# Optimization experiments

Measured on AMD Instinct MI355X. Metric: run time of the kernel, lower is better.

## Reference

```python
import jax, jax.numpy as jnp
import numpy as np

N, E, CS, HE, H = 10000, 160000, 128, 32, 4
S0, V1 = 16, 8          # feat_irreps = 16x0e + 8x1o
QK0, QK1 = 4, 2         # qk_irreps per head = 4x0e + 2x1o
VO0, VO1 = 4, 4         # v_irreps  per head = 4x0e + 4x1o
OK0, OK1 = QK0 * H, QK1 * H     # 16, 8
OV0, OV1 = VO0 * H, VO1 * H     # 16, 16
K_NUMEL = S0*OK0 + V1*OK0 + S0*OK1 + V1*OK1 + V1*OK1   # 640
V_NUMEL = S0*OV0 + V1*OV0 + S0*OV1 + V1*OV1 + V1*OV1   # 896
EPS = 1e-5


def _tp(fs, fv, sh_s, sh_v, w, o0, o1):
    """CG tensor product of (s0 scalars + v1 vectors) with sh=(1x0e+1x1o),
    per-edge weights w (shared_weights=False); outputs o0 scalars + o1 vectors.
    Paths: 0e*0e->0e, 1o.1o->0e (dot), 0e*1o->1o, 1o*0e->1o, 1o x 1o->1o (cross)."""
    s0, v1 = fs.shape[-1], fv.shape[-2]
    i = 0
    ws = []
    for (a, b) in ((s0, o0), (v1, o0), (s0, o1), (v1, o1), (v1, o1)):
        ws.append(w[:, i:i + a * b].reshape(-1, a, b)); i += a * b
    wA, wB, wC, wD, wE = ws
    c0a = jnp.einsum('eu,euw->ew', fs * sh_s[:, None], wA) / np.sqrt(s0)
    dv = jnp.einsum('eui,ei->eu', fv, sh_v)
    c0b = jnp.einsum('eu,euw->ew', dv, wB) / np.sqrt(v1)
    out0 = (c0a + c0b) / np.sqrt(2.0)
    c1c = jnp.einsum('eu,euw->ew', fs, wC)[:, :, None] * sh_v[:, None, :] / np.sqrt(s0)
    c1d = jnp.einsum('eui,euw->ewi', fv, wD) * sh_s[:, None, None] / np.sqrt(v1)
    crs = jnp.cross(fv, sh_v[:, None, :])
    c1e = jnp.einsum('eui,euw->ewi', crs, wE) / np.sqrt(v1)
    out1 = (c1c + c1d + c1e) / np.sqrt(3.0)
    return out0, out1


def _forward(frame_features, rigid_rot, rigid_trans, tfn_features, edge_features, edge_sh,
             W_f0, b_f0, W_f1, b_f1, Wg_s, Wg_v, Wq_s, Wq_v,
             Wk1, bk1, Wk2, bk2, Wv1, bv1, Wv2, bv2,
             Wo_s, Wo_v, Ws_s, Ws_v, bn_ws, bn_bs, bn_wv, edge_index):
    dst, src = edge_index[0], edge_index[1]
    n = tfn_features.shape[0]
    tfn_s = tfn_features[:, :S0]
    tfn_v = tfn_features[:, S0:].reshape(n, V1, 3)
    sh_s, sh_v = edge_sh[:, 0], edge_sh[:, 1:4]

    # frame -> irrep features: 0e via Linear, 1o via Linear + rigid apply
    f0 = frame_features @ W_f0 + b_f0                                   # [N, S0*H]
    f1 = (frame_features @ W_f1 + b_f1).reshape(n, V1 * H, 3)
    f1 = jnp.einsum('nij,nuj->nui', rigid_rot, f1) + rigid_trans[:, None, :]
    gs = f0 @ Wg_s / np.sqrt(f0.shape[-1])                              # o3.Linear 0e -> [N, S0]
    gv = jnp.einsum('nui,uw->nwi', f1, Wg_v) / np.sqrt(f1.shape[1])     # o3.Linear 1o -> [N, V1, 3]

    # queries per node, per head
    q_s = (tfn_s @ Wq_s / np.sqrt(S0)).reshape(n, H, QK0)
    q_v = (jnp.einsum('nui,uw->nwi', tfn_v, Wq_v) / np.sqrt(V1)).reshape(n, H, QK1, 3)

    # per-edge dynamic TP weights from edge features (the big memory term)
    kw = jax.nn.relu(edge_features @ Wk1 + bk1) @ Wk2 + bk2             # [E, 640]
    vw = jax.nn.relu(edge_features @ Wv1 + bv1) @ Wv2 + bv2             # [E, 896]

    fs, fv = gs[dst], gv[dst]                                           # gather at edge_dst
    k_s, k_v = _tp(fs, fv, sh_s, sh_v, kw, OK0, OK1)
    v_s, v_v = _tp(fs, fv, sh_s, sh_v, vw, OV0, OV1)
    k_s = k_s.reshape(-1, H, QK0); k_v = k_v.reshape(-1, H, QK1, 3)
    v_s = v_s.reshape(-1, H, VO0); v_v = v_v.reshape(-1, H, VO1, 3)

    # attention scores + segment softmax over edge_src groups
    attn = jnp.einsum('ehj,ehj->eh', q_s[src], k_s) + jnp.einsum('ehji,ehji->eh', q_v[src], k_v)
    m = jax.ops.segment_max(attn, src, num_segments=n)
    ex = jnp.exp(attn - m[src])
    den = jax.ops.segment_sum(ex, src, num_segments=n)
    alpha = ex / (den[src] + 1e-9)

    upd_s = jax.ops.segment_sum(v_s * alpha[..., None], src, num_segments=n).reshape(n, OV0)
    upd_v = jax.ops.segment_sum(v_v * alpha[..., None, None], src, num_segments=n).reshape(n, OV1, 3)

    out_s = upd_s @ Wo_s / np.sqrt(OV0) + tfn_s @ Ws_s / np.sqrt(S0)
    out_v = jnp.einsum('nui,uw->nwi', upd_v, Wo_v) / np.sqrt(OV1) \
          + jnp.einsum('nui,uw->nwi', tfn_v, Ws_v) / np.sqrt(V1)

    # e3nn-style BatchNorm: scalars mean/var normalized, vectors norm normalized
    mu = out_s.mean(0); xc = out_s - mu
    out_s = xc / jnp.sqrt((xc * xc).mean(0) + EPS) * bn_ws + bn_bs
    n2 = (out_v * out_v).sum(-1).mean(0)
    out_v = out_v / jnp.sqrt(n2 + EPS)[None, :, None] * bn_wv[None, :, None]

    return jnp.concatenate([out_s, out_v.reshape(n, V1 * 3)], axis=-1)   # [N, 40]


def setup_inputs():
    key = jax.random.key(0)
    ks = iter(jax.random.split(key, 40))
    rn = lambda *s: jax.random.normal(next(ks), s, dtype=jnp.float32)
    return dict(
        frame_features=rn(N, CS),
        rigid_rot=rn(N, 3, 3),
        rigid_trans=rn(N, 3),
        tfn_features=rn(N, S0 + 3 * V1),
        edge_features=rn(E, HE),
        edge_sh=rn(E, 4),
        edge_index=jax.random.randint(next(ks), (2, E), 0, N, dtype=jnp.int32),
        W_f0=rn(CS, S0 * H) / np.sqrt(CS), b_f0=jnp.zeros((S0 * H,), jnp.float32),
        W_f1=rn(CS, V1 * H * 3) / np.sqrt(CS), b_f1=jnp.zeros((V1 * H * 3,), jnp.float32),
        Wg_s=rn(S0 * H, S0), Wg_v=rn(V1 * H, V1),
        Wq_s=rn(S0, QK0 * H), Wq_v=rn(V1, QK1 * H),
        Wk1=rn(HE, HE) / np.sqrt(HE), bk1=jnp.zeros((HE,), jnp.float32),
        Wk2=rn(HE, K_NUMEL) / np.sqrt(HE), bk2=jnp.zeros((K_NUMEL,), jnp.float32),
        Wv1=rn(HE, HE) / np.sqrt(HE), bv1=jnp.zeros((HE,), jnp.float32),
        Wv2=rn(HE, V_NUMEL) / np.sqrt(HE), bv2=jnp.zeros((V_NUMEL,), jnp.float32),
        Wo_s=rn(VO0 * H, S0), Wo_v=rn(VO1 * H, V1),
        Ws_s=rn(S0, S0), Ws_v=rn(V1, V1),
        bn_ws=jnp.ones((S0,), jnp.float32), bn_bs=jnp.zeros((S0,), jnp.float32),
        bn_wv=jnp.ones((V1,), jnp.float32),
    )


def reference(frame_features, rigid_rot, rigid_trans, tfn_features, edge_features, edge_sh, edge_index,
              W_f0, b_f0, W_f1, b_f1, Wg_s, Wg_v, Wq_s, Wq_v,
              Wk1, bk1, Wk2, bk2, Wv1, bv1, Wv2, bv2,
              Wo_s, Wo_v, Ws_s, Ws_v, bn_ws, bn_bs, bn_wv):
    return _forward(frame_features, rigid_rot, rigid_trans, tfn_features, edge_features, edge_sh,
                    W_f0, b_f0, W_f1, b_f1, Wg_s, Wg_v, Wq_s, Wq_v,
                    Wk1, bk1, Wk2, bk2, Wv1, bv1, Wv2, bv2,
                    Wo_s, Wo_v, Ws_s, Ws_v, bn_ws, bn_bs, bn_wv, edge_index)
```

## Files before the change

### kernel.cpp

```cpp
#include <hip/hip_runtime.h>
#include <hip/hip_bf16.h>
#include <math.h>

#define NN 10000
#define EE 160000
#define CSZ 128

#define INV_S8  0.35355339059327373f
#define INV_S32 0.17677669529663687f
#define INV_S2  0.7071067811865476f
#define INV_S3  0.5773502691896258f

typedef short s16x8 __attribute__((ext_vector_type(8)));
typedef float f32x4 __attribute__((ext_vector_type(4)));

__device__ __forceinline__ unsigned short f2bf(float f){
  __hip_bfloat16 h = __float2bfloat16(f);
  return *reinterpret_cast<unsigned short*>(&h);
}

__global__ __launch_bounds__(256) void k_f0f1(
    const float* __restrict__ frame,
    const float* __restrict__ Wf0, const float* __restrict__ bf0,
    const float* __restrict__ Wf1, const float* __restrict__ bf1,
    float* __restrict__ f0f1){
  int lane = threadIdx.x & 63, wave = threadIdx.x >> 6;
  int c = blockIdx.x*64 + lane;
  int n0 = blockIdx.y*16 + wave*4;
  if(c >= 160) return;
  bool is0 = c < 64;
  int cc = is0 ? c : (c-64);
  const float* W = is0 ? Wf0 : Wf1;
  int ldw = is0 ? 64 : 96;
  float b = is0 ? bf0[cc] : bf1[cc];
  float acc[4] = {b, b, b, b};
  const float* fp = frame + (size_t)n0*CSZ;
  #pragma unroll 4
  for(int k=0;k<CSZ;k++){
    float w = W[k*ldw + cc];
    #pragma unroll
    for(int j=0;j<4;j++)
      acc[j] = fmaf(fp[j*CSZ + k], w, acc[j]);
  }
  #pragma unroll
  for(int j=0;j<4;j++) f0f1[(size_t)(n0+j)*160 + c] = acc[j];
}

__global__ __launch_bounds__(256) void k_node2(
    const float* __restrict__ f0f1, const float* __restrict__ rot,
    const float* __restrict__ trans, const float* __restrict__ tfn,
    const float* __restrict__ Wgs, const float* __restrict__ Wgv,
    const float* __restrict__ Wqs, const float* __restrict__ Wqv,
    float* __restrict__ Gs, float* __restrict__ Gv,
    float* __restrict__ Qs, float* __restrict__ Qv){
  __shared__ float f1r[4][32][3];
  int ln = threadIdx.x & 63;
  int g  = threadIdx.x >> 6;
  int n  = blockIdx.x*4 + g;
  if(n < NN && ln < 32){
    int u = ln;
    float v0 = f0f1[(size_t)n*160 + 64 + u*3 + 0];
    float v1 = f0f1[(size_t)n*160 + 64 + u*3 + 1];
    float v2 = f0f1[(size_t)n*160 + 64 + u*3 + 2];
    const float* R = rot + (size_t)n*9;
    const float* t = trans + (size_t)n*3;
    f1r[g][u][0] = R[0]*v0 + R[1]*v1 + R[2]*v2 + t[0];
    f1r[g][u][1] = R[3]*v0 + R[4]*v1 + R[5]*v2 + t[1];
    f1r[g][u][2] = R[6]*v0 + R[7]*v1 + R[8]*v2 + t[2];
  }
  __syncthreads();
  if(n >= NN) return;
  if(ln < 16){
    int w = ln; float a = 0.f;
    for(int u=0;u<64;u++) a = fmaf(f0f1[(size_t)n*160+u], Wgs[u*16+w], a);
    Gs[(size_t)n*16+w] = a * 0.125f;
  } else if(ln < 40){
    int idx = ln-16, w = idx/3, i = idx%3; float a = 0.f;
    for(int u=0;u<32;u++) a = fmaf(f1r[g][u][i], Wgv[u*8+w], a);
    Gv[(size_t)n*24+idx] = a * INV_S32;
  }
  if(ln < 16){
    int w = ln; float a = 0.f;
    for(int u=0;u<16;u++) a = fmaf(tfn[(size_t)n*40+u], Wqs[u*16+w], a);
    Qs[(size_t)n*16+w] = a * 0.25f;
  } else if(ln < 40){
    int idx = ln-16, w = idx/3, i = idx%3; float a = 0.f;
    for(int u=0;u<8;u++) a = fmaf(tfn[(size_t)n*40+16+u*3+i], Wqv[u*8+w], a);
    Qv[(size_t)n*24+idx] = a * INV_S8;
  }
}

__global__ __launch_bounds__(256) void k_hist(const int* __restrict__ ei, int* __restrict__ cnt){
  int e = blockIdx.x*256 + threadIdx.x;
  if(e < EE) atomicAdd(&cnt[ei[EE + e]], 1);
}

__global__ __launch_bounds__(256) void k_scan(const int* __restrict__ cnt,
                                              int* __restrict__ ofs, int* __restrict__ fill){
  __shared__ int tsum[256];
  int t = threadIdx.x;
  const int CH = (NN + 255)/256;
  int base = t*CH;
  int s = 0;
  for(int i=0;i<CH;i++){ int idx=base+i; if(idx<NN) s += cnt[idx]; }
  tsum[t] = s;
  __syncthreads();
  for(int off=1; off<256; off<<=1){
    int v = (t>=off)? tsum[t-off] : 0;
    __syncthreads();
    tsum[t] += v;
    __syncthreads();
  }
  int run = (t==0)? 0 : tsum[t-1];
  for(int i=0;i<CH;i++){
    int idx = base+i;
    if(idx < NN){ ofs[idx] = run; fill[idx] = run; run += cnt[idx]; }
  }
  if(t==255) ofs[NN] = tsum[255];
}

__global__ __launch_bounds__(256) void k_scatter(const int* __restrict__ ei,
                                                 int* __restrict__ fill, int* __restrict__ elist){
  int e = blockIdx.x*256 + threadIdx.x;
  if(e >= EE) return;
  int src = ei[EE + e];
  int pos = atomicAdd(&fill[src], 1);
  elist[pos] = e;
}

__global__ __launch_bounds__(256) void k_prepw(
    const float* __restrict__ Wk2, const float* __restrict__ bk2,
    const float* __restrict__ Wv2, const float* __restrict__ bv2,
    unsigned short* __restrict__ A2rK, unsigned short* __restrict__ A2rV,
    float* __restrict__ biasK, float* __restrict__ biasV){
  int tid = blockIdx.x*256 + threadIdx.x;
  const int NV = 896*32, NK = 640*32;
  if(tid < NV){
    int c = tid>>5, h = tid&31;
    float s = (c<384)? INV_S2 : INV_S3;
    A2rV[(c>>4)*512 + (c&15)*32 + h] = f2bf(Wv2[h*896+c]*s);
  } else if(tid < NV+NK){
    int i = tid - NV; int c = i>>5, h = i&31;
    float s = (c<384)? INV_S2 : INV_S3;
    A2rK[(c>>4)*512 + (c&15)*32 + h] = f2bf(Wk2[h*640+c]*s);
  } else if(tid < NV+NK+896){
    int c = tid - (NV+NK);
    biasV[c] = bv2[c] * ((c<384)? INV_S2 : INV_S3);
  } else if(tid < NV+NK+896+640){
    int c = tid - (NV+NK+896);
    biasK[c] = bk2[c] * ((c<384)? INV_S2 : INV_S3);
  }
}

#define HID_TO_FRAGS(W1, b1) { \
  unsigned short* hL = (unsigned short*)&F[0][0]; \
  float efv[32]; \
  const float4* efp = (const float4*)(ef + (size_t)e*32); \
  _Pragma("unroll") \
  for(int q=0;q<8;q++){ float4 t=efp[q]; efv[q*4]=t.x; efv[q*4+1]=t.y; efv[q*4+2]=t.z; efv[q*4+3]=t.w; } \
  float hd[32]; \
  _Pragma("unroll") \
  for(int h=0;h<32;h++) hd[h] = b1[h]; \
  _Pragma("unroll") \
  for(int k=0;k<32;k++){ \
    float ekv = efv[k]; \
    _Pragma("unroll") \
    for(int h=0;h<32;h++) hd[h] = fmaf(ekv, W1[k*32+h], hd[h]); \
  } \
  _Pragma("unroll") \
  for(int gg=0;gg<4;gg++){ \
    s16x8 p; \
    _Pragma("unroll") \
    for(int j=0;j<8;j++) p[j] = (short)f2bf(fmaxf(hd[gg*8+j], 0.f)); \
    *(s16x8*)&hL[((g*4+gg)*16 + e16)*8] = p; \
  } \
  _Pragma("unroll") \
  for(int tt=0;tt<4;tt++) \
    af[tt] = *(const s16x8*)&hL[((tt*4 + g)*16 + e16)*8]; }

#define STAGE_FEATURES() { \
  const float4* g4 = (const float4*)(Gs + (size_t)dst*16); \
  _Pragma("unroll") \
  for(int q=0;q<4;q++){ float4 t = g4[q]; \
    F[q*4+0][lane]=t.x*0.25f; F[q*4+1][lane]=t.y*0.25f; \
    F[q*4+2][lane]=t.z*0.25f; F[q*4+3][lane]=t.w*0.25f; } \
  const float4* v4 = (const float4*)(Gv + (size_t)dst*24); \
  _Pragma("unroll") \
  for(int q=0;q<6;q++){ float4 t = v4[q]; \
    F[16+q*4+0][lane]=t.x; F[16+q*4+1][lane]=t.y; \
    F[16+q*4+2][lane]=t.z; F[16+q*4+3][lane]=t.w; } \
  _Pragma("unroll") \
  for(int tt=0;tt<4;tt++){ \
    int sl = tt*16 + e16; \
    shs_t[tt]  = __shfl(shs, sl); \
    sv_t[tt][0]= __shfl(sv0, sl); \
    sv_t[tt][1]= __shfl(sv1, sl); \
    sv_t[tt][2]= __shfl(sv2, sl); \
    shsI8_t[tt]= shs_t[tt]*INV_S8; \
  } }

#define NTILE_MFMA(A2r, bias, NT) \
  s16x8 Aw = *(const s16x8*)&A2r[(NT)*512 + e16*32 + g*8]; \
  float4 b4 = *(const float4*)&bias[(NT)*16 + g*4]; \
  f32x4 acc4[4]; \
  _Pragma("unroll") \
  for(int tt=0; tt<4; ++tt){ \
    f32x4 a0 = {b4.x, b4.y, b4.z, b4.w}; \
    acc4[tt] = __builtin_amdgcn_mfma_f32_16x16x32_bf16(Aw, af[tt], a0, 0, 0, 0); \
  }

__global__ __launch_bounds__(128) void k_edge_v3(
    const int* __restrict__ ei, const float* __restrict__ esh,
    const float* __restrict__ ef,
    const float* __restrict__ Gs, const float* __restrict__ Gv,
    const float* __restrict__ Wv1, const float* __restrict__ bv1,
    const unsigned short* __restrict__ A2rV, const float* __restrict__ biasV,
    float* __restrict__ EdgeV){
  __shared__ float featAll[2][40][64];
  int wave = threadIdx.x >> 6, lane = threadIdx.x & 63;
  float (*F)[64] = featAll[wave];
  int ebase = blockIdx.x*128 + wave*64;
  int e = ebase + lane;
  int e16 = lane & 15, g = lane >> 4;

  int dst = ei[e];
  float4 sh4 = *(const float4*)(esh + (size_t)e*4);
  float shs = sh4.x, sv0 = sh4.y, sv1 = sh4.z, sv2 = sh4.w;

  s16x8 af[4];
  HID_TO_FRAGS(Wv1, bv1);
  float shs_t[4], sv_t[4][3], shsI8_t[4];
  STAGE_FEATURES();

  float A16[4][4] = {};
  #pragma unroll 1
  for(int ntile=0; ntile<16; ++ntile){
    NTILE_MFMA(A2rV, biasV, ntile);
    #pragma unroll
    for(int tt=0; tt<4; ++tt){
      float f = F[ntile][tt*16+e16] * shs_t[tt];
      #pragma unroll
      for(int r=0;r<4;r++) A16[tt][r] = fmaf(f, acc4[tt][r], A16[tt][r]);
    }
  }
  #pragma unroll 1
  for(int ntile=16; ntile<24; ++ntile){
    NTILE_MFMA(A2rV, biasV, ntile);
    int u3 = 16 + (ntile-16)*3;
    #pragma unroll
    for(int tt=0; tt<4; ++tt){
      int eL = tt*16+e16;
      float f = (F[u3+0][eL]*sv_t[tt][0] + F[u3+1][eL]*sv_t[tt][1]
               + F[u3+2][eL]*sv_t[tt][2]) * INV_S8;
      #pragma unroll
      for(int r=0;r<4;r++) A16[tt][r] = fmaf(f, acc4[tt][r], A16[tt][r]);
    }
  }
  #pragma unroll
  for(int tt=0; tt<4; ++tt){
    int eo = ebase + tt*16 + e16;
    *(float4*)(EdgeV + (size_t)eo*64 + g*4) =
        make_float4(A16[tt][0], A16[tt][1], A16[tt][2], A16[tt][3]);
  }

  float VV[4][4][3] = {};
  #pragma unroll 1
  for(int ntile=24; ntile<40; ++ntile){
    NTILE_MFMA(A2rV, biasV, ntile);
    #pragma unroll
    for(int tt=0; tt<4; ++tt){
      float f = F[ntile-24][tt*16+e16];
      #pragma unroll
      for(int r=0;r<4;r++){
        float c = f*acc4[tt][r];
        VV[tt][r][0] = fmaf(c, sv_t[tt][0], VV[tt][r][0]);
        VV[tt][r][1] = fmaf(c, sv_t[tt][1], VV[tt][r][1]);
        VV[tt][r][2] = fmaf(c, sv_t[tt][2], VV[tt][r][2]);
      }
    }
  }
  #pragma unroll 1
  for(int ntile=40; ntile<48; ++ntile){
    NTILE_MFMA(A2rV, biasV, ntile);
    int u3 = 16 + (ntile-40)*3;
    #pragma unroll
    for(int tt=0; tt<4; ++tt){
      int eL = tt*16+e16;
      float f0 = F[u3+0][eL]*shsI8_t[tt];
      float f1 = F[u3+1][eL]*shsI8_t[tt];
      float f2 = F[u3+2][eL]*shsI8_t[tt];
      #pragma unroll
      for(int r=0;r<4;r++){
        VV[tt][r][0] = fmaf(f0, acc4[tt][r], VV[tt][r][0]);
        VV[tt][r][1] = fmaf(f1, acc4[tt][r], VV[tt][r][1]);
        VV[tt][r][2] = fmaf(f2, acc4[tt][r], VV[tt][r][2]);
      }
    }
  }
  #pragma unroll 1
  for(int ntile=48; ntile<56; ++ntile){
    NTILE_MFMA(A2rV, biasV, ntile);
    int u3 = 16 + (ntile-48)*3;
    #pragma unroll
    for(int tt=0; tt<4; ++tt){
      int eL = tt*16+e16;
      float a0 = F[u3+0][eL], a1 = F[u3+1][eL], a2 = F[u3+2][eL];
      float x0 = (a1*sv_t[tt][2] - a2*sv_t[tt][1])*INV_S8;
      float x1 = (a2*sv_t[tt][0] - a0*sv_t[tt][2])*INV_S8;
      float x2 = (a0*sv_t[tt][1] - a1*sv_t[tt][0])*INV_S8;
      #pragma unroll
      for(int r=0;r<4;r++){
        VV[tt][r][0] = fmaf(x0, acc4[tt][r], VV[tt][r][0]);
        VV[tt][r][1] = fmaf(x1, acc4[tt][r], VV[tt][r][1]);
        VV[tt][r][2] = fmaf(x2, acc4[tt][r], VV[tt][r][2]);
      }
    }
  }
  #pragma unroll
  for(int tt=0; tt<4; ++tt){
    int eo = ebase + tt*16 + e16;
    float* op = EdgeV + (size_t)eo*64 + 16 + g*12;
    float v[12] = {VV[tt][0][0],VV[tt][0][1],VV[tt][0][2],
                   VV[tt][1][0],VV[tt][1][1],VV[tt][1][2],
                   VV[tt][2][0],VV[tt][2][1],VV[tt][2][2],
                   VV[tt][3][0],VV[tt][3][1],VV[tt][3][2]};
    #pragma unroll
    for(int k=0;k<6;k++)
      *(float2*)(op + k*2) = make_float2(v[k*2], v[k*2+1]);
  }
}

__global__ __launch_bounds__(128) void k_edge_k3(
    const int* __restrict__ ei, const float* __restrict__ esh,
    const float* __restrict__ ef,
    const float* __restrict__ Gs, const float* __restrict__ Gv,
    const float* __restrict__ Qs, const float* __restrict__ Qv,
    const float* __restrict__ Wk1, const float* __restrict__ bk1,
    const unsigned short* __restrict__ A2rK, const float* __restrict__ biasK,
    float* __restrict__ Attn){
  __shared__ float featAll[2][40][64];
  int wave = threadIdx.x >> 6, lane = threadIdx.x & 63;
  float (*F)[64] = featAll[wave];
  int ebase = blockIdx.x*128 + wave*64;
  int e = ebase + lane;
  int e16 = lane & 15, g = lane >> 4;

  int dst = ei[e];
  float4 sh4 = *(const float4*)(esh + (size_t)e*4);
  float shs = sh4.x, sv0 = sh4.y, sv1 = sh4.z, sv2 = sh4.w;

  s16x8 af[4];
  HID_TO_FRAGS(Wk1, bk1);
  float shs_t[4], sv_t[4][3], shsI8_t[4];
  STAGE_FEATURES();

  float KS[4][4] = {};
  #pragma unroll 1
  for(int ntile=0; ntile<16; ++ntile){
    NTILE_MFMA(A2rK, biasK, ntile);
    #pragma unroll
    for(int tt=0; tt<4; ++tt){
      float f = F[ntile][tt*16+e16] * shs_t[tt];
      #pragma unroll
      for(int r=0;r<4;r++) KS[tt][r] = fmaf(f, acc4[tt][r], KS[tt][r]);
    }
  }
  #pragma unroll 1
  for(int ntile=16; ntile<24; ++ntile){
    NTILE_MFMA(A2rK, biasK, ntile);
    int u3 = 16 + (ntile-16)*3;
    #pragma unroll
    for(int tt=0; tt<4; ++tt){
      int eL = tt*16+e16;
      float f = (F[u3+0][eL]*sv_t[tt][0] + F[u3+1][eL]*sv_t[tt][1]
               + F[u3+2][eL]*sv_t[tt][2]) * INV_S8;
      #pragma unroll
      for(int r=0;r<4;r++) KS[tt][r] = fmaf(f, acc4[tt][r], KS[tt][r]);
    }
  }
  int src_t[4]; float ksd[4];
  #pragma unroll
  for(int tt=0; tt<4; ++tt){
    int eo = ebase + tt*16 + e16;
    src_t[tt] = ei[EE + eo];
    float4 q4 = *(const float4*)(Qs + (size_t)src_t[tt]*16 + g*4);
    ksd[tt] = q4.x*KS[tt][0] + q4.y*KS[tt][1] + q4.z*KS[tt][2] + q4.w*KS[tt][3];
  }

  float KV[4][4][3] = {};
  int gh = g >> 1;
  #pragma unroll 1
  for(int ntile=24; ntile<32; ++ntile){
    NTILE_MFMA(A2rK, biasK, ntile);
    int fr = (ntile-24)*2 + gh;
    #pragma unroll
    for(int tt=0; tt<4; ++tt){
      float f = F[fr][tt*16+e16];
      #pragma unroll
      for(int r=0;r<4;r++){
        float c = f*acc4[tt][r];
        KV[tt][r][0] = fmaf(c, sv_t[tt][0], KV[tt][r][0]);
        KV[tt][r][1] = fmaf(c, sv_t[tt][1], KV[tt][r][1]);
        KV[tt][r][2] = fmaf(c, sv_t[tt][2], KV[tt][r][2]);
      }
    }
  }
  #pragma unroll 1
  for(int ntile=32; ntile<36; ++ntile){
    NTILE_MFMA(A2rK, biasK, ntile);
    int u3 = 16 + ((ntile-32)*2 + gh)*3;
    #pragma unroll
    for(int tt=0; tt<4; ++tt){
      int eL = tt*16+e16;
      float f0 = F[u3+0][eL]*shsI8_t[tt];
      float f1 = F[u3+1][eL]*shsI8_t[tt];
      float f2 = F[u3+2][eL]*shsI8_t[tt];
      #pragma unroll
      for(int r=0;r<4;r++){
        KV[tt][r][0] = fmaf(f0, acc4[tt][r], KV[tt][r][0]);
        KV[tt][r][1] = fmaf(f1, acc4[tt][r], KV[tt][r][1]);
        KV[tt][r][2] = fmaf(f2, acc4[tt][r], KV[tt][r][2]);
      }
    }
  }
  #pragma unroll 1
  for(int ntile=36; ntile<40; ++ntile){
    NTILE_MFMA(A2rK, biasK, ntile);
    int u3 = 16 + ((ntile-36)*2 + gh)*3;
    #pragma unroll
    for(int tt=0; tt<4; ++tt){
      int eL = tt*16+e16;
      float a0 = F[u3+0][eL], a1 = F[u3+1][eL], a2 = F[u3+2][eL];
      float x0 = (a1*sv_t[tt][2] - a2*sv_t[tt][1])*INV_S8;
      float x1 = (a2*sv_t[tt][0] - a0*sv_t[tt][2])*INV_S8;
      float x2 = (a0*sv_t[tt][1] - a1*sv_t[tt][0])*INV_S8;
      #pragma unroll
      for(int r=0;r<4;r++){
        KV[tt][r][0] = fmaf(x0, acc4[tt][r], KV[tt][r][0]);
        KV[tt][r][1] = fmaf(x1, acc4[tt][r], KV[tt][r][1]);
        KV[tt][r][2] = fmaf(x2, acc4[tt][r], KV[tt][r][2]);
      }
    }
  }
  int godd = g & 1;
  #pragma unroll
  for(int tt=0; tt<4; ++tt){
    const float* qvp = Qv + (size_t)src_t[tt]*24 + godd*12;
    float4 qa = *(const float4*)(qvp);
    float4 qb = *(const float4*)(qvp+4);
    float4 qc = *(const float4*)(qvp+8);
    float kvs0 = qa.x*KV[tt][0][0] + qa.y*KV[tt][0][1] + qa.z*KV[tt][0][2]
               + qa.w*KV[tt][1][0] + qb.x*KV[tt][1][1] + qb.y*KV[tt][1][2];
    float kvs1 = qb.z*KV[tt][2][0] + qb.w*KV[tt][2][1] + qc.x*KV[tt][2][2]
               + qc.y*KV[tt][3][0] + qc.z*KV[tt][3][1] + qc.w*KV[tt][3][2];
    float p0 = ((g==0)? ksd[tt] : 0.f) + (godd? 0.f : kvs0);
    float p1 = ((g==1)? ksd[tt] : 0.f) + (godd? 0.f : kvs1);
    float p2 = ((g==2)? ksd[tt] : 0.f) + (godd? kvs0 : 0.f);
    float p3 = ((g==3)? ksd[tt] : 0.f) + (godd? kvs1 : 0.f);
    p0 += __shfl_xor(p0,16); p0 += __shfl_xor(p0,32);
    p1 += __shfl_xor(p1,16); p1 += __shfl_xor(p1,32);
    p2 += __shfl_xor(p2,16); p2 += __shfl_xor(p2,32);
    p3 += __shfl_xor(p3,16); p3 += __shfl_xor(p3,32);
    if(lane < 16){
      int eo = ebase + tt*16 + lane;
      *(float4*)(Attn + (size_t)eo*4) = make_float4(p0, p1, p2, p3);
    }
  }
}

__global__ __launch_bounds__(256) void k_reduce(
    const int* __restrict__ ofs, const int* __restrict__ elist,
    const float* __restrict__ Attn, const float* __restrict__ EdgeV,
    float* __restrict__ Upd){
  int wid = threadIdx.x >> 6, ln = threadIdx.x & 63;
  int n = blockIdx.x*4 + wid;
  if(n >= NN) return;
  int beg = ofs[n], end = ofs[n+1];
  float m0=-3.4e38f, m1=-3.4e38f, m2=-3.4e38f, m3=-3.4e38f;
  for(int i=beg+ln; i<end; i+=64){
    int e = elist[i];
    float4 a = *(const float4*)(Attn + (size_t)e*4);
    m0=fmaxf(m0,a.x); m1=fmaxf(m1,a.y); m2=fmaxf(m2,a.z); m3=fmaxf(m3,a.w);
  }
  #pragma unroll
  for(int off=1; off<64; off<<=1){
    m0=fmaxf(m0,__shfl_xor(m0,off)); m1=fmaxf(m1,__shfl_xor(m1,off));
    m2=fmaxf(m2,__shfl_xor(m2,off)); m3=fmaxf(m3,__shfl_xor(m3,off));
  }
  int h = (ln < 16) ? (ln >> 2) : (((ln - 16)/3) >> 2);
  float mh = (h==0)?m0:(h==1)?m1:(h==2)?m2:m3;
  float acc = 0.f, den = 0.f;
  for(int i=beg; i<end; i++){
    int e = elist[i];
    float v  = EdgeV[(size_t)e*64 + ln];
    float a  = Attn[(size_t)e*4 + h];
    float ex = __expf(a - mh);
    acc = fmaf(ex, v, acc);
    den += ex;
  }
  Upd[(size_t)n*64 + ln] = acc / (den + 1e-9f);
}

__global__ __launch_bounds__(256) void k_nodeout(
    const float* __restrict__ Upd, const float* __restrict__ tfn,
    const float* __restrict__ Wos, const float* __restrict__ Wov,
    const float* __restrict__ Wss, const float* __restrict__ Wsv,
    float* __restrict__ Pre, float* __restrict__ Stats){
  int n = blockIdx.x*256 + threadIdx.x;
  int lane = threadIdx.x & 63;
  float os[16], ov[24];
  if(n < NN){
    float us[16];
    #pragma unroll
    for(int u=0;u<16;u++) us[u] = Upd[(size_t)n*64+u];
    float uv[48];
    #pragma unroll
    for(int j=0;j<48;j++) uv[j] = Upd[(size_t)n*64+16+j];
    float ts[16];
    #pragma unroll
    for(int u=0;u<16;u++) ts[u] = tfn[(size_t)n*40+u];
    #pragma unroll
    for(int w=0;w<16;w++){
      float a=0.f, b=0.f;
      #pragma unroll
      for(int u=0;u<16;u++){ a = fmaf(us[u], Wos[u*16+w], a); b = fmaf(ts[u], Wss[u*16+w], b); }
      os[w] = (a + b)*0.25f;
    }
    float tv[24];
    #pragma unroll
    for(int j=0;j<24;j++) tv[j] = tfn[(size_t)n*40+16+j];
    #pragma unroll
    for(int w=0;w<8;w++){
      #pragma unroll
      for(int i=0;i<3;i++){
        float a=0.f;
        #pragma unroll
        for(int u=0;u<16;u++) a = fmaf(uv[u*3+i], Wov[u*8+w], a);
        float b=0.f;
        #pragma unroll
        for(int u=0;u<8;u++) b = fmaf(tv[u*3+i], Wsv[u*8+w], b);
        ov[w*3+i] = a*0.25f + b*INV_S8;
      }
    }
    float* p = Pre + (size_t)n*40;
    #pragma unroll
    for(int w=0;w<16;w++) p[w] = os[w];
    #pragma unroll
    for(int j=0;j<24;j++) p[16+j] = ov[j];
  } else {
    #pragma unroll
    for(int w=0;w<16;w++) os[w]=0.f;
    #pragma unroll
    for(int j=0;j<24;j++) ov[j]=0.f;
  }
#define WAVE_RED_ADD(v) { v += __shfl_xor(v,1); v += __shfl_xor(v,2); v += __shfl_xor(v,4); \
                          v += __shfl_xor(v,8); v += __shfl_xor(v,16); v += __shfl_xor(v,32); }
  #pragma unroll
  for(int c=0;c<16;c++){
    float s = os[c];       WAVE_RED_ADD(s);
    float q = os[c]*os[c]; WAVE_RED_ADD(q);
    if(lane==0){ atomicAdd(&Stats[c], s); atomicAdd(&Stats[16+c], q); }
  }
  #pragma unroll
  for(int w=0;w<8;w++){
    float q = ov[w*3]*ov[w*3] + ov[w*3+1]*ov[w*3+1] + ov[w*3+2]*ov[w*3+2];
    WAVE_RED_ADD(q);
    if(lane==0) atomicAdd(&Stats[32+w], q);
  }
#undef WAVE_RED_ADD
}

__global__ __launch_bounds__(256) void k_final(
    const float* __restrict__ Pre, const float* __restrict__ Stats,
    const float* __restrict__ bnws, const float* __restrict__ bnbs,
    const float* __restrict__ bnwv, float* __restrict__ Out){
  int idx = blockIdx.x*256 + threadIdx.x;
  if(idx >= NN*40) return;
  int n = idx/40, c = idx - n*40;
  float x = Pre[idx];
  float r;
  if(c < 16){
    float mu  = Stats[c]    * (1.f/NN);
    float var = Stats[16+c] * (1.f/NN) - mu*mu;
    r = (x - mu) / sqrtf(var + 1e-5f) * bnws[c] + bnbs[c];
  } else {
    int w = (c-16)/3;
    float n2 = Stats[32+w] * (1.f/NN);
    r = x / sqrtf(n2 + 1e-5f) * bnwv[w];
  }
  Out[idx] = r;
}

extern "C" void kernel_launch(void* const* d_in, const int* in_sizes, int n_in,
                              void* d_out, int out_size, void* d_ws, size_t ws_size,
                              hipStream_t stream){
  const float* frame = (const float*)d_in[0];
  const float* rot   = (const float*)d_in[1];
  const float* trans = (const float*)d_in[2];
  const float* tfn   = (const float*)d_in[3];
  const float* ef    = (const float*)d_in[4];
  const float* esh   = (const float*)d_in[5];
  const int*   ei    = (const int*)  d_in[6];
  const float* Wf0   = (const float*)d_in[7];
  const float* bf0   = (const float*)d_in[8];
  const float* Wf1   = (const float*)d_in[9];
  const float* bf1   = (const float*)d_in[10];
  const float* Wgs   = (const float*)d_in[11];
  const float* Wgv   = (const float*)d_in[12];
  const float* Wqs   = (const float*)d_in[13];
  const float* Wqv   = (const float*)d_in[14];
  const float* Wk1   = (const float*)d_in[15];
  const float* bk1   = (const float*)d_in[16];
  const float* Wk2   = (const float*)d_in[17];
  const float* bk2   = (const float*)d_in[18];
  const float* Wv1   = (const float*)d_in[19];
  const float* bv1   = (const float*)d_in[20];
  const float* Wv2   = (const float*)d_in[21];
  const float* bv2   = (const float*)d_in[22];
  const float* Wos   = (const float*)d_in[23];
  const float* Wov   = (const float*)d_in[24];
  const float* Wss   = (const float*)d_in[25];
  const float* Wsv   = (const float*)d_in[26];
  const float* bnws  = (const float*)d_in[27];
  const float* bnbs  = (const float*)d_in[28];
  const float* bnwv  = (const float*)d_in[29];

  float* ws   = (float*)d_ws;
  float* f0f1 = ws;
  float* Gs   = f0f1 + (size_t)NN*160;
  float* Gv   = Gs   + (size_t)NN*16;
  float* Qs   = Gv   + (size_t)NN*24;
  float* Qv   = Qs   + (size_t)NN*16;
  float* Attn = Qv   + (size_t)NN*24;
  float* Pre  = Attn + (size_t)EE*4;
  float* Upd  = Pre  + (size_t)NN*40;
  float* EdgeV= Upd  + (size_t)NN*64;
  float* Stats= EdgeV+ (size_t)EE*64;
  int*   cnt  = (int*)(Stats + 64);
  int*   ofs  = cnt + (NN+16);
  int*   fill = ofs + (NN+16);
  int*   elist= fill + (NN+16);
  float* biasV= (float*)(elist + EE);
  float* biasK= biasV + 896;
  unsigned short* A2rV = (unsigned short*)(biasK + 640);
  unsigned short* A2rK = A2rV + 896*32;

  hipMemsetAsync(Stats, 0, (64 + NN + 16)*sizeof(int), stream);

  k_f0f1    <<<dim3(3, NN/16),        256, 0, stream>>>(frame, Wf0, bf0, Wf1, bf1, f0f1);
  k_prepw   <<<dim3(198),             256, 0, stream>>>(Wk2, bk2, Wv2, bv2, A2rK, A2rV, biasK, biasV);
  k_node2   <<<dim3(NN/4),            256, 0, stream>>>(f0f1, rot, trans, tfn, Wgs, Wgv, Wqs, Wqv, Gs, Gv, Qs, Qv);
  k_hist    <<<dim3((EE+255)/256),    256, 0, stream>>>(ei, cnt);
  k_scan    <<<dim3(1),               256, 0, stream>>>(cnt, ofs, fill);
  k_scatter <<<dim3((EE+255)/256),    256, 0, stream>>>(ei, fill, elist);
  k_edge_v3 <<<dim3(EE/128),          128, 0, stream>>>(ei, esh, ef, Gs, Gv, Wv1, bv1, A2rV, biasV, EdgeV);
  k_edge_k3 <<<dim3(EE/128),          128, 0, stream>>>(ei, esh, ef, Gs, Gv, Qs, Qv, Wk1, bk1, A2rK, biasK, Attn);
  k_reduce  <<<dim3((NN+3)/4),        256, 0, stream>>>(ofs, elist, Attn, EdgeV, Upd);
  k_nodeout <<<dim3((NN+255)/256),    256, 0, stream>>>(Upd, tfn, Wos, Wov, Wss, Wsv, Pre, Stats);
  k_final   <<<dim3((NN*40+255)/256), 256, 0, stream>>>(Pre, Stats, bnws, bnbs, bnwv, (float*)d_out);
}
```

Measured before the change: 302.2 us.

## Parallelize node output projection across lanes per output channel with LDS staging

```diff
diff --git a/kernel.cpp b/kernel.cpp
--- a/kernel.cpp
+++ b/kernel.cpp
@@ -506,68 +506,65 @@
     const float* __restrict__ Wos, const float* __restrict__ Wov,
     const float* __restrict__ Wss, const float* __restrict__ Wsv,
     float* __restrict__ Pre, float* __restrict__ Stats){
-  int n = blockIdx.x*256 + threadIdx.x;
-  int lane = threadIdx.x & 63;
-  float os[16], ov[24];
-  if(n < NN){
-    float us[16];
-    #pragma unroll
-    for(int u=0;u<16;u++) us[u] = Upd[(size_t)n*64+u];
-    float uv[48];
-    #pragma unroll
-    for(int j=0;j<48;j++) uv[j] = Upd[(size_t)n*64+16+j];
-    float ts[16];
-    #pragma unroll
-    for(int u=0;u<16;u++) ts[u] = tfn[(size_t)n*40+u];
-    #pragma unroll
-    for(int w=0;w<16;w++){
+  __shared__ float sbuf[4][104];
+  int wave = threadIdx.x >> 6, lane = threadIdx.x & 63;
+  int n0 = (blockIdx.x*4 + wave)*4;
+  int c = lane;
+  float Wa[16], Wb[16];
+  if(c < 16){
+    #pragma unroll
+    for(int u=0;u<16;u++){ Wa[u]=Wos[u*16+c]; Wb[u]=Wss[u*16+c]; }
+  } else if(c < 40){
+    int w = (c-16)/3;
+    #pragma unroll
+    for(int u=0;u<16;u++) Wa[u]=Wov[u*8+w];
+    #pragma unroll
+    for(int u=0;u<8;u++)  Wb[u]=Wsv[u*8+w];
+  }
+  float S1 = 0.f, S2 = 0.f;
+  #pragma unroll 1
+  for(int j=0;j<4;j++){
+    int n = n0 + j;
+    if(n >= NN) break;
+    sbuf[wave][lane] = Upd[(size_t)n*64 + lane];
+    if(lane < 40) sbuf[wave][64+lane] = tfn[(size_t)n*40 + lane];
+    if(c < 16){
       float a=0.f, b=0.f;
       #pragma unroll
-      for(int u=0;u<16;u++){ a = fmaf(us[u], Wos[u*16+w], a); b = fmaf(ts[u], Wss[u*16+w], b); }
-      os[w] = (a + b)*0.25f;
-    }
-    float tv[24];
-    #pragma unroll
-    for(int j=0;j<24;j++) tv[j] = tfn[(size_t)n*40+16+j];
-    #pragma unroll
-    for(int w=0;w<8;w++){
-      #pragma unroll
-      for(int i=0;i<3;i++){
-        float a=0.f;
-        #pragma unroll
-        for(int u=0;u<16;u++) a = fmaf(uv[u*3+i], Wov[u*8+w], a);
-        float b=0.f;
-        #pragma unroll
-        for(int u=0;u<8;u++) b = fmaf(tv[u*3+i], Wsv[u*8+w], b);
-        ov[w*3+i] = a*0.25f + b*INV_S8;
+      for(int u=0;u<16;u++){
+        a = fmaf(sbuf[wave][u],    Wa[u], a);
+        b = fmaf(sbuf[wave][64+u], Wb[u], b);
       }
-    }
-    float* p = Pre + (size_t)n*40;
-    #pragma unroll
-    for(int w=0;w<16;w++) p[w] = os[w];
-    #pragma unroll
-    for(int j=0;j<24;j++) p[16+j] = ov[j];
-  } else {
-    #pragma unroll
-    for(int w=0;w<16;w++) os[w]=0.f;
-    #pragma unroll
-    for(int j=0;j<24;j++) ov[j]=0.f;
-  }
-#define WAVE_RED_ADD(v) { v += __shfl_xor(v,1); v += __shfl_xor(v,2); v += __shfl_xor(v,4); \
-                          v += __shfl_xor(v,8); v += __shfl_xor(v,16); v += __shfl_xor(v,32); }
-  #pragma unroll
-  for(int c=0;c<16;c++){
-    float s = os[c];       WAVE_RED_ADD(s);
-    float q = os[c]*os[c]; WAVE_RED_ADD(q);
-    if(lane==0){ atomicAdd(&Stats[c], s); atomicAdd(&Stats[16+c], q); }
-  }
-  #pragma unroll
-  for(int w=0;w<8;w++){
-    float q = ov[w*3]*ov[w*3] + ov[w*3+1]*ov[w*3+1] + ov[w*3+2]*ov[w*3+2];
-    WAVE_RED_ADD(q);
-    if(lane==0) atomicAdd(&Stats[32+w], q);
-  }
-#undef WAVE_RED_ADD
+      float out = (a+b)*0.25f;
+      S1 += out; S2 += out*out;
+      Pre[(size_t)n*40+c] = out;
+    } else if(c < 40){
+      int i = (c-16)%3;
+      float a=0.f, b=0.f;
+      #pragma unroll
+      for(int u=0;u<16;u++) a = fmaf(sbuf[wave][16+u*3+i],    Wa[u], a);
+      #pragma unroll
+      for(int u=0;u<8;u++)  b = fmaf(sbuf[wave][64+16+u*3+i], Wb[u], b);
+      float out = a*0.25f + b*INV_S8;
+      S1 += out*out;
+      Pre[(size_t)n*40+c] = out;
+    }
+  }
+  __syncthreads();
+  if(lane < 40) sbuf[wave][lane]    = S1;
+  if(lane < 16) sbuf[wave][40+lane] = S2;
+  __syncthreads();
+  if(wave == 0){
+    if(lane < 40){
+      float t = sbuf[0][lane]+sbuf[1][lane]+sbuf[2][lane]+sbuf[3][lane];
+      if(lane < 16) atomicAdd(&Stats[lane], t);
+      else          atomicAdd(&Stats[32+(lane-16)/3], t);
+    }
+    if(lane < 16){
+      float t2 = sbuf[0][40+lane]+sbuf[1][40+lane]+sbuf[2][40+lane]+sbuf[3][40+lane];
+      atomicAdd(&Stats[16+lane], t2);
+    }
+  }
 }
 
 __global__ __launch_bounds__(256) void k_final(
@@ -656,6 +653,6 @@
   k_edge_v3 <<<dim3(EE/128),          128, 0, stream>>>(ei, esh, ef, Gs, Gv, Wv1, bv1, A2rV, biasV, EdgeV);
   k_edge_k3 <<<dim3(EE/128),          128, 0, stream>>>(ei, esh, ef, Gs, Gv, Qs, Qv, Wk1, bk1, A2rK, biasK, Attn);
   k_reduce  <<<dim3((NN+3)/4),        256, 0, stream>>>(ofs, elist, Attn, EdgeV, Upd);
-  k_nodeout <<<dim3((NN+255)/256),    256, 0, stream>>>(Upd, tfn, Wos, Wov, Wss, Wsv, Pre, Stats);
+  k_nodeout <<<dim3((NN+15)/16),      256, 0, stream>>>(Upd, tfn, Wos, Wov, Wss, Wsv, Pre, Stats);
   k_final   <<<dim3((NN*40+255)/256), 256, 0, stream>>>(Pre, Stats, bnws, bnbs, bnwv, (float*)d_out);
 }
```

Measured after the change: 343.9 us. +13.8%, slower.
